# Kernel tuning notes

Hardware: AMD Instinct MI355X
Metric: run time of the kernel (lower is better)

The kernel has to match this reference:

```python
import jax, jax.numpy as jnp
import numpy as np

ALG_DIM = 248   # dim of E8 adjoint rep
NNZ = 30000     # number of nonzero structure constants f_{ij}^k
BATCH = 8192


def setup_inputs() -> dict:
    key = jax.random.key(0)
    k1, k2, k3, k4, k5, k6 = jax.random.split(key, 6)
    x = jax.random.normal(k1, (BATCH, ALG_DIM), dtype=jnp.float32)
    y = jax.random.normal(k2, (BATCH, ALG_DIM), dtype=jnp.float32)
    idx_i = jax.random.randint(k3, (NNZ,), 0, ALG_DIM, dtype=jnp.int32)
    idx_j = jax.random.randint(k4, (NNZ,), 0, ALG_DIM, dtype=jnp.int32)
    idx_k = jax.random.randint(k5, (NNZ,), 0, ALG_DIM, dtype=jnp.int32)
    coeff = jax.random.normal(k6, (NNZ,), dtype=jnp.float32)
    alpha = jnp.ones((1,), dtype=jnp.float32)
    return {"x": x, "y": y, "idx_i": idx_i, "idx_j": idx_j,
            "idx_k": idx_k, "coeff": coeff, "alpha": alpha}


def reference(x, y, idx_i, idx_j, idx_k, coeff, alpha):
    # Sparse Lie bracket via structure-constant triples:
    #   out[b, k] = sum_{t : idx_k[t]==k} coeff[t] * x[b, idx_i[t]] * y[b, idx_j[t]]
    vals = x[:, idx_i] * y[:, idx_j] * coeff[None, :]          # (B, nnz)
    bracket = jnp.zeros_like(x).at[:, idx_k].add(vals)          # (B, 248)
    return alpha[0] * bracket
```

## Files before the change

kernel.cpp:

```cpp
#include <hip/hip_runtime.h>

#define ALG_DIM 248
#define ROWS 32
#define KSPLIT 4
#define KPB 62
#define CAP 256
#define CNT_STRIDE 16
#define PLSTRIDE_B 3984
#define PLSTRIDE_DW 996

typedef __fp16 h2v __attribute__((ext_vector_type(2)));
union H2U { unsigned u; h2v h; };


__global__ void k_scatter(const int* __restrict__ idx_i, const int* __restrict__ idx_j,
                          const int* __restrict__ idx_k, const float* __restrict__ coeff,
                          int* __restrict__ cnt, uint2* __restrict__ packed, int nnz) {
    const int t = blockIdx.x * 256 + threadIdx.x;
    if (t >= nnz) return;
    const int k = idx_k[t];
    const int pos = atomicAdd(&cnt[k * CNT_STRIDE], 1);
    if (pos < CAP) {
        const float c = coeff[t];
        H2U hc; hc.h = __builtin_amdgcn_cvt_pkrtz(c, c);
        uint2 p;
        p.x = ((unsigned)idx_i[t] << 4) | ((unsigned)idx_j[t] << 20);
        p.y = hc.u;
        packed[((size_t)k << 8) + pos] = p;
    }
}


__global__ __launch_bounds__(256, 4) void k_main(
    const float* __restrict__ x, const float* __restrict__ y,
    const uint4* __restrict__ packed4,
    const int* __restrict__ cnt,
    const float* __restrict__ alpha_p, float* __restrict__ out)
{
    __shared__ __align__(16) unsigned xs32[4 * PLSTRIDE_DW];
    __shared__ __align__(16) unsigned ys32[4 * PLSTRIDE_DW];

    const int tid = threadIdx.x;
    const int r0  = blockIdx.x * ROWS;

    for (int u = tid; u < (ALG_DIM / 4) * (ROWS / 2); u += 256) {
        const int rp = u & 15;
        const int cq = u >> 4;
        const size_t ra = (size_t)(r0 + 2 * rp) * ALG_DIM + 4 * cq;
        const float4 xa = *reinterpret_cast<const float4*>(x + ra);
        const float4 xb = *reinterpret_cast<const float4*>(x + ra + ALG_DIM);
        const float4 ya = *reinterpret_cast<const float4*>(y + ra);
        const float4 yb = *reinterpret_cast<const float4*>(y + ra + ALG_DIM);
        const int pbase = (rp >> 2) * PLSTRIDE_DW + (rp & 3);
#define STG(d, XA, XB, YA, YB)                                                  \
        {                                                                       \
            const int dw = pbase + (4 * cq + (d)) * 4;                          \
            H2U hx; hx.h = __builtin_amdgcn_cvt_pkrtz(XA, XB);                  \
            H2U hy; hy.h = __builtin_amdgcn_cvt_pkrtz(YA, YB);                  \
            xs32[dw] = hx.u;                                                    \
            ys32[dw] = hy.u;                                                    \
        }
        STG(0, xa.x, xb.x, ya.x, yb.x)
        STG(1, xa.y, xb.y, ya.y, yb.y)
        STG(2, xa.z, xb.z, ya.z, yb.z)
        STG(3, xa.w, xb.w, ya.w, yb.w)
#undef STG
    }
    __syncthreads();

    const float alpha = alpha_p[0];
    const int   S     = tid >> 2;
    const int   q     = tid & 3;

    const char* xsb = reinterpret_cast<const char*>(xs32) + q * PLSTRIDE_B;
    const char* ysb = reinterpret_cast<const char*>(ys32) + q * PLSTRIDE_B;

    if (S < KPB) {
        const int p  = blockIdx.y * KPB + S;
        const int k  = p;
        const int sz = min(cnt[p * CNT_STRIDE], CAP);
        const uint4* tp = packed4 + ((size_t)p << 7);

        float a0 = 0.f, a1 = 0.f, a2 = 0.f, a3 = 0.f,
              a4 = 0.f, a5 = 0.f, a6 = 0.f, a7 = 0.f;

        const int nFull = sz >> 1;
        uint4 cur = tp[0];

#define PROC(PW, PC)                                                            \
        {                                                                       \
            const unsigned ox = (PW) & 0xFFFFu;                                 \
            const unsigned oy = (PW) >> 16;                                     \
            const uint4 wx = *reinterpret_cast<const uint4*>(xsb + ox);         \
            const uint4 wy = *reinterpret_cast<const uint4*>(ysb + oy);         \
            H2U cc; cc.u = (PC);                                                \
            H2U ux, uy;                                                         \
            ux.u = wx.x; uy.u = wy.x; c0 = (ux.h * uy.h) * cc.h + c0;           \
            ux.u = wx.y; uy.u = wy.y; c1 = (ux.h * uy.h) * cc.h + c1;           \
            ux.u = wx.z; uy.u = wy.z; c2 = (ux.h * uy.h) * cc.h + c2;           \
            ux.u = wx.w; uy.u = wy.w; c3 = (ux.h * uy.h) * cc.h + c3;           \
        }
#define FLUSH                                                                   \
        a0 += (float)c0.x; a1 += (float)c0.y;                                   \
        a2 += (float)c1.x; a3 += (float)c1.y;                                   \
        a4 += (float)c2.x; a5 += (float)c2.y;                                   \
        a6 += (float)c3.x; a7 += (float)c3.y;

        for (int chunk = 0; chunk < nFull; chunk += 16) {
            h2v c0 = (h2v)0.0f, c1 = (h2v)0.0f, c2 = (h2v)0.0f, c3 = (h2v)0.0f;
            const int hend = min(chunk + 16, nFull);
#pragma unroll 2
            for (int h = chunk; h < hend; ++h) {
                const uint4 nxt = tp[h + 1];
                PROC(cur.x, cur.y)
                PROC(cur.z, cur.w)
                cur = nxt;
            }
            FLUSH
        }
        if (sz & 1) {
            h2v c0 = (h2v)0.0f, c1 = (h2v)0.0f, c2 = (h2v)0.0f, c3 = (h2v)0.0f;
            PROC(cur.x, cur.y)
            FLUSH
        }
#undef FLUSH
#undef PROC

        const int rbase = r0 + (q << 3);
        out[(size_t)(rbase + 0) * ALG_DIM + k] = alpha * a0;
        out[(size_t)(rbase + 1) * ALG_DIM + k] = alpha * a1;
        out[(size_t)(rbase + 2) * ALG_DIM + k] = alpha * a2;
        out[(size_t)(rbase + 3) * ALG_DIM + k] = alpha * a3;
        out[(size_t)(rbase + 4) * ALG_DIM + k] = alpha * a4;
        out[(size_t)(rbase + 5) * ALG_DIM + k] = alpha * a5;
        out[(size_t)(rbase + 6) * ALG_DIM + k] = alpha * a6;
        out[(size_t)(rbase + 7) * ALG_DIM + k] = alpha * a7;
    }
}


extern "C" void kernel_launch(void* const* d_in, const int* in_sizes, int n_in,
                              void* d_out, int out_size, void* d_ws, size_t ws_size,
                              hipStream_t stream) {
    const float* x      = (const float*)d_in[0];
    const float* y      = (const float*)d_in[1];
    const int*   idx_i  = (const int*)d_in[2];
    const int*   idx_j  = (const int*)d_in[3];
    const int*   idx_k  = (const int*)d_in[4];
    const float* coeff  = (const float*)d_in[5];
    const float* alpha  = (const float*)d_in[6];
    float*       out    = (float*)d_out;

    const int nnz   = in_sizes[2];
    const int batch = in_sizes[0] / ALG_DIM;

    char*  ws     = (char*)d_ws;
    int*   cnt    = (int*)ws;
    uint2* packed = (uint2*)(ws + 16384);

    hipMemsetAsync(ws, 0, 16384, stream);

    k_scatter<<<(nnz + 255) / 256, 256, 0, stream>>>(idx_i, idx_j, idx_k, coeff,
                                                     cnt, packed, nnz);

    dim3 grid(batch / ROWS, KSPLIT);
    k_main<<<grid, 256, 0, stream>>>(x, y, (const uint4*)packed, cnt, alpha, out);
}
```

Measured before the change: 107.0 us.

## Process two column groups per block to reuse staged x/y tiles

Halves the number of column splits so each block stages its 32 rows of x and y into shared memory once and then runs two gather-accumulate passes over different output columns. Count and first packed-entry loads are issued before the staging loop to overlap their latency. This reduces redundant global reads and fp16 conversion of x/y, at the cost of fewer blocks and longer serial work per block.

```diff
diff --git a/kernel.cpp b/kernel.cpp
--- a/kernel.cpp
+++ b/kernel.cpp
@@ -2,7 +2,8 @@
 
 #define ALG_DIM 248
 #define ROWS 32
-#define KSPLIT 4
+#define KSPLIT 2
+#define KPH 124
 #define KPB 62
 #define CAP 256
 #define CNT_STRIDE 16
@@ -42,6 +43,21 @@
 
     const int tid = threadIdx.x;
     const int r0  = blockIdx.x * ROWS;
+    const int y2  = blockIdx.y;
+
+    const int S = tid >> 2;
+    const int q = tid & 3;
+    const bool act = (S < KPB);
+
+    const int pA = y2 * KPH + ((S < KPB) ? S : 0);
+    const int pB = pA + KPB;
+    const uint4* tpA = packed4 + ((size_t)pA << 7);
+    const uint4* tpB = packed4 + ((size_t)pB << 7);
+    const int szA = act ? min(cnt[pA * CNT_STRIDE], CAP) : 0;
+    const int szB = act ? min(cnt[pB * CNT_STRIDE], CAP) : 0;
+    uint4 primeA = tpA[0];
+    uint4 primeB = tpB[0];
+    const float alpha = alpha_p[0];
 
     for (int u = tid; u < (ALG_DIM / 4) * (ROWS / 2); u += 256) {
         const int rp = u & 15;
@@ -68,24 +84,9 @@
     }
     __syncthreads();
 
-    const float alpha = alpha_p[0];
-    const int   S     = tid >> 2;
-    const int   q     = tid & 3;
-
     const char* xsb = reinterpret_cast<const char*>(xs32) + q * PLSTRIDE_B;
     const char* ysb = reinterpret_cast<const char*>(ys32) + q * PLSTRIDE_B;
-
-    if (S < KPB) {
-        const int p  = blockIdx.y * KPB + S;
-        const int k  = p;
-        const int sz = min(cnt[p * CNT_STRIDE], CAP);
-        const uint4* tp = packed4 + ((size_t)p << 7);
-
-        float a0 = 0.f, a1 = 0.f, a2 = 0.f, a3 = 0.f,
-              a4 = 0.f, a5 = 0.f, a6 = 0.f, a7 = 0.f;
-
-        const int nFull = sz >> 1;
-        uint4 cur = tp[0];
+    const int rbase = r0 + (q << 3);
 
 #define PROC(PW, PC)                                                            \
         {                                                                       \
@@ -106,36 +107,45 @@
         a4 += (float)c2.x; a5 += (float)c2.y;                                   \
         a6 += (float)c3.x; a7 += (float)c3.y;
 
-        for (int chunk = 0; chunk < nFull; chunk += 16) {
-            h2v c0 = (h2v)0.0f, c1 = (h2v)0.0f, c2 = (h2v)0.0f, c3 = (h2v)0.0f;
-            const int hend = min(chunk + 16, nFull);
-#pragma unroll 2
-            for (int h = chunk; h < hend; ++h) {
-                const uint4 nxt = tp[h + 1];
-                PROC(cur.x, cur.y)
-                PROC(cur.z, cur.w)
-                cur = nxt;
-            }
-            FLUSH
-        }
-        if (sz & 1) {
-            h2v c0 = (h2v)0.0f, c1 = (h2v)0.0f, c2 = (h2v)0.0f, c3 = (h2v)0.0f;
-            PROC(cur.x, cur.y)
-            FLUSH
-        }
+#define GATHER_STORE(TP, SZ, PRIME, K)                                          \
+    if (act) {                                                                  \
+        float a0 = 0.f, a1 = 0.f, a2 = 0.f, a3 = 0.f,                           \
+              a4 = 0.f, a5 = 0.f, a6 = 0.f, a7 = 0.f;                           \
+        const int nFull = (SZ) >> 1;                                            \
+        uint4 cur = (PRIME);                                                    \
+        for (int chunk = 0; chunk < nFull; chunk += 16) {                       \
+            h2v c0 = (h2v)0.0f, c1 = (h2v)0.0f, c2 = (h2v)0.0f, c3 = (h2v)0.0f; \
+            const int hend = min(chunk + 16, nFull);                            \
+            _Pragma("unroll 2")                                                 \
+            for (int h = chunk; h < hend; ++h) {                                \
+                const uint4 nxt = (TP)[h + 1];                                  \
+                PROC(cur.x, cur.y)                                              \
+                PROC(cur.z, cur.w)                                              \
+                cur = nxt;                                                      \
+            }                                                                   \
+            FLUSH                                                               \
+        }                                                                       \
+        if ((SZ) & 1) {                                                         \
+            h2v c0 = (h2v)0.0f, c1 = (h2v)0.0f, c2 = (h2v)0.0f, c3 = (h2v)0.0f; \
+            PROC(cur.x, cur.y)                                                  \
+            FLUSH                                                               \
+        }                                                                       \
+        out[(size_t)(rbase + 0) * ALG_DIM + (K)] = alpha * a0;                  \
+        out[(size_t)(rbase + 1) * ALG_DIM + (K)] = alpha * a1;                  \
+        out[(size_t)(rbase + 2) * ALG_DIM + (K)] = alpha * a2;                  \
+        out[(size_t)(rbase + 3) * ALG_DIM + (K)] = alpha * a3;                  \
+        out[(size_t)(rbase + 4) * ALG_DIM + (K)] = alpha * a4;                  \
+        out[(size_t)(rbase + 5) * ALG_DIM + (K)] = alpha * a5;                  \
+        out[(size_t)(rbase + 6) * ALG_DIM + (K)] = alpha * a6;                  \
+        out[(size_t)(rbase + 7) * ALG_DIM + (K)] = alpha * a7;                  \
+    }
+
+    GATHER_STORE(tpA, szA, primeA, pA)
+    GATHER_STORE(tpB, szB, primeB, pB)
+
+#undef GATHER_STORE
 #undef FLUSH
 #undef PROC
-
-        const int rbase = r0 + (q << 3);
-        out[(size_t)(rbase + 0) * ALG_DIM + k] = alpha * a0;
-        out[(size_t)(rbase + 1) * ALG_DIM + k] = alpha * a1;
-        out[(size_t)(rbase + 2) * ALG_DIM + k] = alpha * a2;
-        out[(size_t)(rbase + 3) * ALG_DIM + k] = alpha * a3;
-        out[(size_t)(rbase + 4) * ALG_DIM + k] = alpha * a4;
-        out[(size_t)(rbase + 5) * ALG_DIM + k] = alpha * a5;
-        out[(size_t)(rbase + 6) * ALG_DIM + k] = alpha * a6;
-        out[(size_t)(rbase + 7) * ALG_DIM + k] = alpha * a7;
-    }
 }
 
 
```

After: 108.4 us. Within noise of the previous version (+1.3%).
